# Performance work log

Measured on AMD Instinct MI355X. Metric: run time of the kernel, lower is better.

## Reference

```python
import jax, jax.numpy as jnp
import numpy as np

H = 4096
I = 11008
S = 4096
B = 1


def _swiglu_mlp(x, Wgu, Wd):
    # x: [B, T, H]; Wgu: [H, 2I]; Wd: [I, H]
    gu = jnp.einsum('bth,hi->bti', x, Wgu)
    gate, up = gu[..., :I], gu[..., I:]
    return jnp.einsum('bti,ih->bth', jax.nn.silu(gate) * up, Wd)


def setup_inputs() -> dict:
    key = jax.random.key(0)
    ks = jax.random.split(key, 5)
    scale_h = 1.0 / np.sqrt(H)
    scale_i = 1.0 / np.sqrt(I)
    hidden_states = jax.random.normal(ks[0], (B, S, H), dtype=jnp.float32)
    lang_ids = jnp.arange(S // 2, dtype=jnp.int64 if jax.config.jax_enable_x64 else jnp.int32)
    vision_ids = jnp.arange(S // 2, S, dtype=lang_ids.dtype)
    Wgu_lang = jax.random.normal(ks[1], (H, 2 * I), dtype=jnp.float32) * scale_h
    Wd_lang = jax.random.normal(ks[2], (I, H), dtype=jnp.float32) * scale_i
    Wgu_vis = jax.random.normal(ks[3], (H, 2 * I), dtype=jnp.float32) * scale_h
    Wd_vis = jax.random.normal(ks[4], (I, H), dtype=jnp.float32) * scale_i
    return {
        'hidden_states': hidden_states,
        'lang_ids': lang_ids,
        'vision_ids': vision_ids,
        'Wgu_lang': Wgu_lang,
        'Wd_lang': Wd_lang,
        'Wgu_vis': Wgu_vis,
        'Wd_vis': Wd_vis,
    }


def reference(hidden_states, lang_ids, vision_ids, Wgu_lang, Wd_lang, Wgu_vis, Wd_vis):
    # gather-by-token-type -> SwiGLU MLP per expert -> scatter-combine
    lang_out = _swiglu_mlp(hidden_states[:, lang_ids], Wgu_lang, Wd_lang)
    vis_out = _swiglu_mlp(hidden_states[:, vision_ids], Wgu_vis, Wd_vis)
    out = jnp.zeros_like(hidden_states)
    out = out.at[:, lang_ids].set(lang_out)
    out = out.at[:, vision_ids].set(vis_out)
    return out
```

## Files before the change

### kernel.cpp

```cpp
#include <hip/hip_runtime.h>
#include <hip/hip_bf16.h>


#define HDIM 4096
#define IDIM 11008
#define N2   22016
#define MTOK 2048
#define KT1  64
#define KT2  172
#define NB1  86
#define NB2  32
#define NKD  344
#define NPG  128

#define XPE_SH ((long)8 * KT1 * 16384)
#define WPE_SH ((long)NB1 * KT1 * 16384)
#define HPE_SH ((long)8 * KT2 * 16384)

typedef unsigned short ushort_t;
using f32x4  = __attribute__((ext_vector_type(4))) float;
using bf16x8 = __attribute__((ext_vector_type(8))) short;
using u32x2  = __attribute__((ext_vector_type(2))) unsigned int;
using u32x4  = __attribute__((ext_vector_type(4))) unsigned int;

__device__ __forceinline__ unsigned int bf16rne(float f) {
    unsigned int u = __builtin_bit_cast(unsigned int, f);
    return (u + 0x7FFFu + ((u >> 16) & 1u)) >> 16;
}
__device__ __forceinline__ unsigned int pack2(float lo, float hi) {
    return bf16rne(lo) | (bf16rne(hi) << 16);
}
__device__ __forceinline__ void gl_lds16(const void* g, void* l) {
    __builtin_amdgcn_global_load_lds(
        (const __attribute__((address_space(1))) void*)g,
        (__attribute__((address_space(3))) void*)l, 16, 0, 0);
}


__global__ __launch_bounds__(256)
void conv_x(const float* __restrict__ X, ushort_t* __restrict__ XP) {
    int bid = blockIdx.x;
    int mb = bid >> 6, kt = bid & 63;
    int t = threadIdx.x;
    int r0 = t >> 4, c4 = t & 15;
    int kh = c4 >> 3, c = (c4 >> 1) & 3, lo4 = (c4 & 1) << 2;
    ushort_t* tp = XP + ((long)(mb >> 1) * KT1 + kt) * 16384 + (long)kh * 8192 + (mb & 1) * 4096;
#pragma unroll
    for (int p = 0; p < 8; ++p) {
        int rl = r0 + p * 16;
        f32x4 v = *(const f32x4*)(X + (long)(mb * 128 + rl) * HDIM + kt * 64 + c4 * 4);
        u32x2 pk = { pack2(v[0], v[1]), pack2(v[2], v[3]) };
        int q = rl >> 1;
        int pos = ((((rl & 1) << 2) | c) ^ (q & 7));
        *(u32x2*)&tp[q * 64 + pos * 8 + lo4] = pk;
    }
}

__global__ __launch_bounds__(256)
void conv_wgu(const float* __restrict__ W, ushort_t* __restrict__ WP) {
    int bid = blockIdx.x;
    int e = bid & 1, kt = (bid >> 1) & 63, nb = bid >> 7;
    int t = threadIdx.x;
    int kp = t >> 5, c4 = t & 31;
    const float* p = W + ((long)kt * 64 + kp * 8) * N2 + (long)e * IDIM + nb * 128 + c4 * 4;
    f32x4 v[8];
#pragma unroll
    for (int j = 0; j < 8; ++j) v[j] = *(const f32x4*)(p + (long)j * N2);
    ushort_t* tp = WP + ((long)nb * KT1 + kt) * 16384 + (long)(kp >> 2) * 8192 + e * 4096;
    int c = kp & 3;
#pragma unroll
    for (int cc = 0; cc < 4; ++cc) {
        int n = c4 * 4 + cc;
        int q = n >> 1;
        int pos = ((((n & 1) << 2) | c) ^ (q & 7));
        u32x4 pk = { pack2(v[0][cc], v[1][cc]), pack2(v[2][cc], v[3][cc]),
                     pack2(v[4][cc], v[5][cc]), pack2(v[6][cc], v[7][cc]) };
        *(u32x4*)&tp[q * 64 + pos * 8] = pk;
    }
}

__global__ __launch_bounds__(256)
void conv_wd2b(const float* __restrict__ Wl, const float* __restrict__ Wv,
               ushort_t* __restrict__ WPd) {
    int bid = blockIdx.x;
    int kt = bid % KT2, nbp = bid / KT2;
    int e = nbp >> 4, nb = nbp & 15;
    const float* W = e ? Wv : Wl;
    int t = threadIdx.x;
    int kp = t >> 5, c4 = t & 31;
    ushort_t* tp = WPd + ((long)nbp * KT2 + kt) * 16384 + (long)(kp >> 2) * 8192;
    int c = kp & 3;
#pragma unroll
    for (int h = 0; h < 2; ++h) {
        const float* p = W + ((long)kt * 64 + kp * 8) * HDIM + nb * 256 + h * 128 + c4 * 4;
        f32x4 v[8];
#pragma unroll
        for (int j = 0; j < 8; ++j) v[j] = *(const f32x4*)(p + (long)j * HDIM);
#pragma unroll
        for (int cc = 0; cc < 4; ++cc) {
            int n = h * 128 + c4 * 4 + cc;
            int q = n >> 1;
            int pos = ((((n & 1) << 2) | c) ^ (q & 7));
            u32x4 pk = { pack2(v[0][cc], v[1][cc]), pack2(v[2][cc], v[3][cc]),
                         pack2(v[4][cc], v[5][cc]), pack2(v[6][cc], v[7][cc]) };
            *(u32x4*)&tp[q * 64 + pos * 8] = pk;
        }
    }
}

__global__ __launch_bounds__(256)
void conv_wd(const float* __restrict__ W, ushort_t* __restrict__ WP) {
    int bid = blockIdx.x;
    int kt = bid % KT2, nb = bid / KT2;
    int t = threadIdx.x;
    int kp = t >> 5, c4 = t & 31;
    const float* p = W + ((long)kt * 64 + kp * 8) * HDIM + nb * 128 + c4 * 4;
    f32x4 v[8];
#pragma unroll
    for (int j = 0; j < 8; ++j) v[j] = *(const f32x4*)(p + (long)j * HDIM);
    ushort_t* tp = WP + ((long)nb * KT2 + kt) * 8192 + (long)(kp >> 2) * 4096;
    int c = kp & 3;
#pragma unroll
    for (int cc = 0; cc < 4; ++cc) {
        int n = c4 * 4 + cc;
        int q = n >> 1;
        int pos = ((((n & 1) << 2) | c) ^ (q & 7));
        u32x4 pk = { pack2(v[0][cc], v[1][cc]), pack2(v[2][cc], v[3][cc]),
                     pack2(v[4][cc], v[5][cc]), pack2(v[6][cc], v[7][cc]) };
        *(u32x4*)&tp[q * 64 + pos * 8] = pk;
    }
}

#define STAGE_U(SRC, DSTOFF) do { \
    gl_lds16((SRC) + so + lane * 8, &lds[(DSTOFF) + so]); \
    gl_lds16((SRC) + 4096 + so + lane * 8, &lds[(DSTOFF) + 4096 + so]); } while (0)

#define MFMA16(ACC, AF, BF) \
    _Pragma("unroll") \
    for (int mf = 0; mf < 4; ++mf) \
        _Pragma("unroll") \
        for (int nf = 0; nf < 4; ++nf) \
            ACC[mf][nf] = __builtin_amdgcn_mfma_f32_16x16x32_bf16(AF[mf], BF[nf], ACC[mf][nf], 0, 0, 0);

#define VMCNT_MID(N) do { \
    if (pf) asm volatile("s_waitcnt vmcnt(" #N ")" ::: "memory"); \
    else    asm volatile("s_waitcnt vmcnt(0)" ::: "memory"); } while (0)
#define VMCNT_END(N) do { \
    if (pf) asm volatile("s_waitcnt vmcnt(" #N ")" ::: "memory"); } while (0)

__global__ __launch_bounds__(512, 2)
void gu15_kernel(const ushort_t* __restrict__ XP, const ushort_t* __restrict__ WP,
                 ushort_t* __restrict__ HP, int perE) {
    __shared__ ushort_t lds[49152];
    int nwg = gridDim.x;
    int cpx = nwg >> 3;
    int sw  = (blockIdx.x & 7) * cpx + (blockIdx.x >> 3);
    int e   = (sw >= perE) ? 1 : 0;
    int lsw = sw - e * perE;
    int mblk = lsw & 7;
    int nblk = lsw >> 3;
    const int t = threadIdx.x, lane = t & 63, w = t >> 6;
    const int wr = w >> 1, wc = w & 1;
    const int rr = lane & 15, g4 = lane >> 4;
    const int so = w * 512;

    int aoff[4], boff[4];
#pragma unroll
    for (int mf = 0; mf < 4; ++mf) {
        int m = wr * 64 + mf * 16 + rr, q = m >> 1;
        aoff[mf] = q * 64 + ((((((m & 1) << 2) | g4) ^ (q & 7))) << 3);
    }
#pragma unroll
    for (int nf = 0; nf < 4; ++nf) {
        int n = wc * 64 + nf * 16 + rr, q = n >> 1;
        boff[nf] = q * 64 + ((((((n & 1) << 2) | g4) ^ (q & 7))) << 3);
    }

    f32x4 accg[4][4] = {}, accu[4][4] = {};
    const ushort_t* srcA = XP + (long)e * XPE_SH + (long)mblk * KT1 * 16384;
    const ushort_t* srcB = WP + (long)e * WPE_SH + (long)nblk * KT1 * 16384;
    ushort_t* HPe = HP + (long)e * HPE_SH;

    STAGE_U(srcA, 0);
    STAGE_U(srcB, 8192);
    STAGE_U(srcA + 8192, 16384);
    STAGE_U(srcB + 8192, 16384 + 8192);
    asm volatile("s_waitcnt vmcnt(4)" ::: "memory");
    __builtin_amdgcn_s_barrier();

    int cb = 0, sb = 32768;
    for (int kt = 0; kt < NPG; ++kt) {
        bf16x8 af[4], bg[4], bu[4];
#pragma unroll
        for (int mf = 0; mf < 4; ++mf) af[mf] = *(const bf16x8*)&lds[cb + aoff[mf]];
#pragma unroll
        for (int nf = 0; nf < 4; ++nf) {
            bg[nf] = *(const bf16x8*)&lds[cb + 8192 + boff[nf]];
            bu[nf] = *(const bf16x8*)&lds[cb + 8192 + 4096 + boff[nf]];
        }
        const bool pf = (kt + 2 < NPG);
        if (pf) {
            const ushort_t* nA = srcA + (long)(kt + 2) * 8192;
            const ushort_t* nB = srcB + (long)(kt + 2) * 8192;
            STAGE_U(nA, sb);
            STAGE_U(nB, sb + 8192);
        }
        __builtin_amdgcn_s_setprio(1);
        MFMA16(accg, af, bg);
        MFMA16(accu, af, bu);
        __builtin_amdgcn_s_setprio(0);
        if (pf)                   asm volatile("s_waitcnt vmcnt(4)" ::: "memory");
        else if (kt + 1 < NPG)    asm volatile("s_waitcnt vmcnt(0)" ::: "memory");
        __builtin_amdgcn_s_barrier();
        sb = cb;
        cb += 16384; if (cb == 49152) cb = 0;
    }

#pragma unroll
    for (int nf = 0; nf < 4; ++nf) {
        int nloc = wc * 64 + nf * 16 + rr;
        int kt2 = nblk * 2 + (nloc >> 6);
        int k = nloc & 63;
        int kh = k >> 5, c = (k >> 3) & 3, klow = k & 7;
        ushort_t* tp = HPe + ((long)mblk * KT2 + kt2) * 16384 + kh * 8192 + klow;
#pragma unroll
        for (int mf = 0; mf < 4; ++mf)
#pragma unroll
            for (int i = 0; i < 4; ++i) {
                int m = wr * 64 + mf * 16 + g4 * 4 + i;
                int q = m >> 1;
                int pos = ((((m & 1) << 2) | c) ^ (q & 7));
                float gv = accg[mf][nf][i], uv = accu[mf][nf][i];
                float s = gv / (1.0f + __expf(-gv));
                tp[q * 64 + pos * 8] = (ushort_t)bf16rne(s * uv);
            }
    }
}

__global__ __launch_bounds__(512, 2)
void down6_kernel(const ushort_t* __restrict__ HP, const ushort_t* __restrict__ WPd,
                  float* __restrict__ Out) {
    __shared__ ushort_t lds[49152];
    int nwg = gridDim.x;
    int cpx = nwg >> 3;
    int sw  = (blockIdx.x & 7) * cpx + (blockIdx.x >> 3);
    int mblk = sw & 15;
    int nblk = sw >> 4;
    const int t = threadIdx.x, lane = t & 63, w = t >> 6;
    const int wr = w >> 2, wc = w & 3;
    const int rr = lane & 15, g4 = lane >> 4;
    const int so = w * 512;

    int aoff[8], boff[4];
#pragma unroll
    for (int mf = 0; mf < 8; ++mf) {
        int m = wr * 128 + mf * 16 + rr, q = m >> 1;
        aoff[mf] = q * 64 + ((((((m & 1) << 2) | g4) ^ (q & 7))) << 3);
    }
#pragma unroll
    for (int nf = 0; nf < 4; ++nf) {
        int n = wc * 64 + nf * 16 + rr, q = n >> 1;
        boff[nf] = q * 64 + ((((((n & 1) << 2) | g4) ^ (q & 7))) << 3);
    }

    f32x4 acc[8][4] = {};
    const ushort_t* srcA = HP  + (long)mblk * KT2 * 16384;
    const ushort_t* srcB = WPd + (long)(((mblk >> 3) << 4) + nblk) * KT2 * 16384;

    STAGE_U(srcA, 0);
    STAGE_U(srcB, 8192);
    STAGE_U(srcA + 8192, 16384);
    STAGE_U(srcB + 8192, 16384 + 8192);
    asm volatile("s_waitcnt vmcnt(4)" ::: "memory");
    __builtin_amdgcn_s_barrier();

    int cb = 0, sb = 32768;
    for (int kt = 0; kt < NKD; ++kt) {
        bf16x8 af[8], bf[4];
#pragma unroll
        for (int mf = 0; mf < 8; ++mf) af[mf] = *(const bf16x8*)&lds[cb + aoff[mf]];
#pragma unroll
        for (int nf = 0; nf < 4; ++nf) bf[nf] = *(const bf16x8*)&lds[cb + 8192 + boff[nf]];
        const bool pf = (kt + 2 < NKD);
        if (pf) {
            const ushort_t* nA = srcA + (long)(kt + 2) * 8192;
            const ushort_t* nB = srcB + (long)(kt + 2) * 8192;
            STAGE_U(nA, sb);
            STAGE_U(nB, sb + 8192);
        }
        __builtin_amdgcn_s_setprio(1);
#pragma unroll
        for (int mf = 0; mf < 8; ++mf)
#pragma unroll
            for (int nf = 0; nf < 4; ++nf)
                acc[mf][nf] = __builtin_amdgcn_mfma_f32_16x16x32_bf16(af[mf], bf[nf], acc[mf][nf], 0, 0, 0);
        __builtin_amdgcn_s_setprio(0);
        if (pf)                   asm volatile("s_waitcnt vmcnt(4)" ::: "memory");
        else if (kt + 1 < NKD)    asm volatile("s_waitcnt vmcnt(0)" ::: "memory");
        __builtin_amdgcn_s_barrier();
        sb = cb;
        cb += 16384; if (cb == 49152) cb = 0;
    }

#pragma unroll
    for (int mf = 0; mf < 8; ++mf)
#pragma unroll
        for (int nf = 0; nf < 4; ++nf)
#pragma unroll
            for (int i = 0; i < 4; ++i) {
                int m = mblk * 256 + wr * 128 + mf * 16 + g4 * 4 + i;
                int n = nblk * 256 + wc * 64 + nf * 16 + rr;
                Out[(long)m * HDIM + n] = acc[mf][nf][i];
            }
}

__global__ __launch_bounds__(512, 2)
void down3_kernel(const ushort_t* __restrict__ HP, const ushort_t* __restrict__ WP,
                  float* __restrict__ Out) {
    __shared__ ushort_t lds[49152];
    int nwg = gridDim.x;
    int cpx = nwg >> 3;
    int sw  = (blockIdx.x & 7) * cpx + (blockIdx.x >> 3);
    int mblk = sw & 7;
    int nblk = sw >> 3;
    const int t = threadIdx.x, lane = t & 63, w = t >> 6;
    const int wr = w >> 1, wc = w & 1;
    const int rr = lane & 15, g4 = lane >> 4;
    const int so = w * 512;

    int aoff[4], boff[4];
#pragma unroll
    for (int mf = 0; mf < 4; ++mf) {
        int m = wr * 64 + mf * 16 + rr, q = m >> 1;
        aoff[mf] = q * 64 + ((((((m & 1) << 2) | g4) ^ (q & 7))) << 3);
    }
#pragma unroll
    for (int nf = 0; nf < 4; ++nf) {
        int n = wc * 64 + nf * 16 + rr, q = n >> 1;
        boff[nf] = q * 64 + ((((((n & 1) << 2) | g4) ^ (q & 7))) << 3);
    }

    f32x4 acc[4][4] = {};
    const ushort_t* srcA = HP + (long)mblk * KT2 * 16384;
    const ushort_t* srcB = WP + (long)nblk * KT2 * 8192;

    STAGE_U(srcA, 0);
    STAGE_U(srcA + 8192, 8192);
    STAGE_U(srcB, 16384);
    asm volatile("s_waitcnt vmcnt(0)" ::: "memory");
    __builtin_amdgcn_s_barrier();

    int cur = 0;
    for (int kt = 0; kt < KT2; ++kt) {
        const int cb = cur * 24576, pb = (cur ^ 1) * 24576;
        const ushort_t* nA = srcA + (long)(kt + 1) * 16384;
        const ushort_t* nB = srcB + (long)(kt + 1) * 8192;
        const bool pf = (kt + 1 < KT2);
        bf16x8 af[4], bfr[4];

#pragma unroll
        for (int mf = 0; mf < 4; ++mf) af[mf] = *(const bf16x8*)&lds[cb + aoff[mf]];
#pragma unroll
        for (int nf = 0; nf < 4; ++nf) bfr[nf] = *(const bf16x8*)&lds[cb + 16384 + boff[nf]];
        if (pf) { STAGE_U(nA, pb); STAGE_U(nB, pb + 16384); }
        __builtin_amdgcn_s_barrier();
        __builtin_amdgcn_s_setprio(1);
        MFMA16(acc, af, bfr);
        __builtin_amdgcn_s_setprio(0);
        VMCNT_MID(4);
        __builtin_amdgcn_s_barrier();

#pragma unroll
        for (int mf = 0; mf < 4; ++mf) af[mf] = *(const bf16x8*)&lds[cb + 8192 + aoff[mf]];
#pragma unroll
        for (int nf = 0; nf < 4; ++nf) bfr[nf] = *(const bf16x8*)&lds[cb + 20480 + boff[nf]];
        if (pf) STAGE_U(nA + 8192, pb + 8192);
        __builtin_amdgcn_s_barrier();
        __builtin_amdgcn_s_setprio(1);
        MFMA16(acc, af, bfr);
        __builtin_amdgcn_s_setprio(0);
        VMCNT_END(2);
        __builtin_amdgcn_s_barrier();

        cur ^= 1;
    }

#pragma unroll
    for (int mf = 0; mf < 4; ++mf)
#pragma unroll
        for (int nf = 0; nf < 4; ++nf)
#pragma unroll
            for (int i = 0; i < 4; ++i) {
                int m = mblk * 256 + wr * 64 + mf * 16 + g4 * 4 + i;
                int n = nblk * 128 + wc * 64 + nf * 16 + rr;
                Out[(long)m * HDIM + n] = acc[mf][nf][i];
            }
}

extern "C" void kernel_launch(void* const* d_in, const int* in_sizes, int n_in,
                              void* d_out, int out_size, void* d_ws, size_t ws_size,
                              hipStream_t stream) {
    const float* x     = (const float*)d_in[0];
    const float* Wgu_l = (const float*)d_in[3];
    const float* Wd_l  = (const float*)d_in[4];
    const float* Wgu_v = (const float*)d_in[5];
    const float* Wd_v  = (const float*)d_in[6];
    float* out         = (float*)d_out;

    const size_t XP_B  = (size_t)8 * KT1 * 32768;
    const size_t HP_B  = (size_t)8 * KT2 * 32768;
    const size_t WP_B  = (size_t)NB1 * KT1 * 32768;
    const size_t NEED0 = 2 * XP_B + 2 * HP_B + 2 * WP_B;
    const size_t NEED1 = XP_B + 2 * HP_B + WP_B;

    if (ws_size >= NEED0) {
        ushort_t* XP = (ushort_t*)d_ws;
        ushort_t* HP = XP + 2 * XPE_SH;
        ushort_t* WP = HP + 2 * HPE_SH;
        for (int e = 0; e < 2; ++e) {
            conv_x  <<<dim3(16 * KT1),      dim3(256), 0, stream>>>(
                x + (long)e * MTOK * HDIM, XP + (long)e * XPE_SH);
            conv_wgu<<<dim3(NB1 * KT1 * 2), dim3(256), 0, stream>>>(
                e ? Wgu_v : Wgu_l, WP + (long)e * WPE_SH);
        }
        gu15_kernel<<<dim3(16 * NB1), dim3(512), 0, stream>>>(XP, WP, HP, 8 * NB1);
        conv_wd2b<<<dim3(32 * KT2), dim3(256), 0, stream>>>(Wd_l, Wd_v, WP);
        down6_kernel<<<dim3(256), dim3(512), 0, stream>>>(HP, WP, out);
    } else if (ws_size >= NEED1) {
        ushort_t* XP = (ushort_t*)d_ws;
        ushort_t* HP = XP + XPE_SH;
        ushort_t* WP = HP + 2 * HPE_SH;
        for (int e = 0; e < 2; ++e) {
            conv_x  <<<dim3(16 * KT1),      dim3(256), 0, stream>>>(
                x + (long)e * MTOK * HDIM, XP);
            conv_wgu<<<dim3(NB1 * KT1 * 2), dim3(256), 0, stream>>>(
                e ? Wgu_v : Wgu_l, WP);
            gu15_kernel<<<dim3(8 * NB1), dim3(512), 0, stream>>>(
                XP, WP, HP + (long)e * HPE_SH, 8 * NB1);
        }
        conv_wd2b<<<dim3(32 * KT2), dim3(256), 0, stream>>>(Wd_l, Wd_v, WP);
        down6_kernel<<<dim3(256), dim3(512), 0, stream>>>(HP, WP, out);
    } else {
        ushort_t* XP = (ushort_t*)d_ws;
        ushort_t* HP = XP + XPE_SH;
        ushort_t* WP = HP + HPE_SH;
        for (int e = 0; e < 2; ++e) {
            const float* xe = x + (long)e * MTOK * HDIM;
            float*       oe = out + (long)e * MTOK * HDIM;
            conv_x  <<<dim3(16 * KT1),      dim3(256), 0, stream>>>(xe, XP);
            conv_wgu<<<dim3(NB1 * KT1 * 2), dim3(256), 0, stream>>>(e ? Wgu_v : Wgu_l, WP);
            gu15_kernel<<<dim3(8 * NB1),    dim3(512), 0, stream>>>(XP, WP, HP, 8 * NB1);
            conv_wd <<<dim3(NB2 * KT2),     dim3(256), 0, stream>>>(e ? Wd_v : Wd_l, WP);
            down3_kernel<<<dim3(8 * NB2),   dim3(512), 0, stream>>>(HP, WP, oe);
        }
    }
}
```

Measured before the change: 1.228 ms.

## Switch GEMM pipelines to double-buffered two-subtile stages with half the barriers

The gate-up and down GEMM kernels move from a 3-slot ring of 32-wide K subtiles (one barrier per subtile, prefetch depth 2) to two 64-wide K buffers. Each loop iteration computes two subtiles, prefetches the next full tile into the other buffer, then waits with vmcnt(0) and a barrier. This halves the number of barriers and waitcnt points. The cost is more LDS per block (128KB), which could lower occupancy, and a shallower prefetch distance, which gives less latency hiding.

Result: slower. 1.254 ms (+2.1%).

```diff
diff --git a/kernel.cpp b/kernel.cpp
--- a/kernel.cpp
+++ b/kernel.cpp
@@ -10,8 +10,6 @@
 #define KT2  172
 #define NB1  86
 #define NB2  32
-#define NKD  344
-#define NPG  128
 
 #define XPE_SH ((long)8 * KT1 * 16384)
 #define WPE_SH ((long)NB1 * KT1 * 16384)
@@ -135,6 +133,12 @@
     gl_lds16((SRC) + so + lane * 8, &lds[(DSTOFF) + so]); \
     gl_lds16((SRC) + 4096 + so + lane * 8, &lds[(DSTOFF) + 4096 + so]); } while (0)
 
+#define STAGE_TILE(NA, NB, PB) do { \
+    STAGE_U((NA), (PB)); \
+    STAGE_U((NB), (PB) + 8192); \
+    STAGE_U((NA) + 8192, (PB) + 16384); \
+    STAGE_U((NB) + 8192, (PB) + 24576); } while (0)
+
 #define MFMA16(ACC, AF, BF) \
     _Pragma("unroll") \
     for (int mf = 0; mf < 4; ++mf) \
@@ -149,9 +153,9 @@
     if (pf) asm volatile("s_waitcnt vmcnt(" #N ")" ::: "memory"); } while (0)
 
 __global__ __launch_bounds__(512, 2)
-void gu15_kernel(const ushort_t* __restrict__ XP, const ushort_t* __restrict__ WP,
+void gu16_kernel(const ushort_t* __restrict__ XP, const ushort_t* __restrict__ WP,
                  ushort_t* __restrict__ HP, int perE) {
-    __shared__ ushort_t lds[49152];
+    __shared__ ushort_t lds[65536];
     int nwg = gridDim.x;
     int cpx = nwg >> 3;
     int sw  = (blockIdx.x & 7) * cpx + (blockIdx.x >> 3);
@@ -181,16 +185,15 @@
     const ushort_t* srcB = WP + (long)e * WPE_SH + (long)nblk * KT1 * 16384;
     ushort_t* HPe = HP + (long)e * HPE_SH;
 
-    STAGE_U(srcA, 0);
-    STAGE_U(srcB, 8192);
-    STAGE_U(srcA + 8192, 16384);
-    STAGE_U(srcB + 8192, 16384 + 8192);
-    asm volatile("s_waitcnt vmcnt(4)" ::: "memory");
+    STAGE_TILE(srcA, srcB, 0);
+    asm volatile("s_waitcnt vmcnt(0)" ::: "memory");
     __builtin_amdgcn_s_barrier();
 
-    int cb = 0, sb = 32768;
-    for (int kt = 0; kt < NPG; ++kt) {
+    for (int tt = 0; tt < KT1; ++tt) {
+        const int cb = (tt & 1) << 15;
+        const int pb = cb ^ 32768;
         bf16x8 af[4], bg[4], bu[4];
+
 #pragma unroll
         for (int mf = 0; mf < 4; ++mf) af[mf] = *(const bf16x8*)&lds[cb + aoff[mf]];
 #pragma unroll
@@ -198,22 +201,30 @@
             bg[nf] = *(const bf16x8*)&lds[cb + 8192 + boff[nf]];
             bu[nf] = *(const bf16x8*)&lds[cb + 8192 + 4096 + boff[nf]];
         }
-        const bool pf = (kt + 2 < NPG);
-        if (pf) {
-            const ushort_t* nA = srcA + (long)(kt + 2) * 8192;
-            const ushort_t* nB = srcB + (long)(kt + 2) * 8192;
-            STAGE_U(nA, sb);
-            STAGE_U(nB, sb + 8192);
+        if (tt + 1 < KT1) {
+            const ushort_t* nA = srcA + (long)(tt + 1) * 16384;
+            const ushort_t* nB = srcB + (long)(tt + 1) * 16384;
+            STAGE_TILE(nA, nB, pb);
         }
         __builtin_amdgcn_s_setprio(1);
         MFMA16(accg, af, bg);
         MFMA16(accu, af, bu);
         __builtin_amdgcn_s_setprio(0);
-        if (pf)                   asm volatile("s_waitcnt vmcnt(4)" ::: "memory");
-        else if (kt + 1 < NPG)    asm volatile("s_waitcnt vmcnt(0)" ::: "memory");
-        __builtin_amdgcn_s_barrier();
-        sb = cb;
-        cb += 16384; if (cb == 49152) cb = 0;
+
+#pragma unroll
+        for (int mf = 0; mf < 4; ++mf) af[mf] = *(const bf16x8*)&lds[cb + 16384 + aoff[mf]];
+#pragma unroll
+        for (int nf = 0; nf < 4; ++nf) {
+            bg[nf] = *(const bf16x8*)&lds[cb + 24576 + boff[nf]];
+            bu[nf] = *(const bf16x8*)&lds[cb + 24576 + 4096 + boff[nf]];
+        }
+        __builtin_amdgcn_s_setprio(1);
+        MFMA16(accg, af, bg);
+        MFMA16(accu, af, bu);
+        __builtin_amdgcn_s_setprio(0);
+
+        asm volatile("s_waitcnt vmcnt(0)" ::: "memory");
+        __builtin_amdgcn_s_barrier();
     }
 
 #pragma unroll
@@ -238,9 +249,9 @@
 }
 
 __global__ __launch_bounds__(512, 2)
-void down6_kernel(const ushort_t* __restrict__ HP, const ushort_t* __restrict__ WPd,
+void down8_kernel(const ushort_t* __restrict__ HP, const ushort_t* __restrict__ WPd,
                   float* __restrict__ Out) {
-    __shared__ ushort_t lds[49152];
+    __shared__ ushort_t lds[65536];
     int nwg = gridDim.x;
     int cpx = nwg >> 3;
     int sw  = (blockIdx.x & 7) * cpx + (blockIdx.x >> 3);
@@ -267,26 +278,23 @@
     const ushort_t* srcA = HP  + (long)mblk * KT2 * 16384;
     const ushort_t* srcB = WPd + (long)(((mblk >> 3) << 4) + nblk) * KT2 * 16384;
 
-    STAGE_U(srcA, 0);
-    STAGE_U(srcB, 8192);
-    STAGE_U(srcA + 8192, 16384);
-    STAGE_U(srcB + 8192, 16384 + 8192);
-    asm volatile("s_waitcnt vmcnt(4)" ::: "memory");
+    STAGE_TILE(srcA, srcB, 0);
+    asm volatile("s_waitcnt vmcnt(0)" ::: "memory");
     __builtin_amdgcn_s_barrier();
 
-    int cb = 0, sb = 32768;
-    for (int kt = 0; kt < NKD; ++kt) {
+    for (int tt = 0; tt < KT2; ++tt) {
+        const int cb = (tt & 1) << 15;
+        const int pb = cb ^ 32768;
         bf16x8 af[8], bf[4];
+
 #pragma unroll
         for (int mf = 0; mf < 8; ++mf) af[mf] = *(const bf16x8*)&lds[cb + aoff[mf]];
 #pragma unroll
         for (int nf = 0; nf < 4; ++nf) bf[nf] = *(const bf16x8*)&lds[cb + 8192 + boff[nf]];
-        const bool pf = (kt + 2 < NKD);
-        if (pf) {
-            const ushort_t* nA = srcA + (long)(kt + 2) * 8192;
-            const ushort_t* nB = srcB + (long)(kt + 2) * 8192;
-            STAGE_U(nA, sb);
-            STAGE_U(nB, sb + 8192);
+        if (tt + 1 < KT2) {
+            const ushort_t* nA = srcA + (long)(tt + 1) * 16384;
+            const ushort_t* nB = srcB + (long)(tt + 1) * 16384;
+            STAGE_TILE(nA, nB, pb);
         }
         __builtin_amdgcn_s_setprio(1);
 #pragma unroll
@@ -295,11 +303,21 @@
             for (int nf = 0; nf < 4; ++nf)
                 acc[mf][nf] = __builtin_amdgcn_mfma_f32_16x16x32_bf16(af[mf], bf[nf], acc[mf][nf], 0, 0, 0);
         __builtin_amdgcn_s_setprio(0);
-        if (pf)                   asm volatile("s_waitcnt vmcnt(4)" ::: "memory");
-        else if (kt + 1 < NKD)    asm volatile("s_waitcnt vmcnt(0)" ::: "memory");
-        __builtin_amdgcn_s_barrier();
-        sb = cb;
-        cb += 16384; if (cb == 49152) cb = 0;
+
+#pragma unroll
+        for (int mf = 0; mf < 8; ++mf) af[mf] = *(const bf16x8*)&lds[cb + 16384 + aoff[mf]];
+#pragma unroll
+        for (int nf = 0; nf < 4; ++nf) bf[nf] = *(const bf16x8*)&lds[cb + 24576 + boff[nf]];
+        __builtin_amdgcn_s_setprio(1);
+#pragma unroll
+        for (int mf = 0; mf < 8; ++mf)
+#pragma unroll
+            for (int nf = 0; nf < 4; ++nf)
+                acc[mf][nf] = __builtin_amdgcn_mfma_f32_16x16x32_bf16(af[mf], bf[nf], acc[mf][nf], 0, 0, 0);
+        __builtin_amdgcn_s_setprio(0);
+
+        asm volatile("s_waitcnt vmcnt(0)" ::: "memory");
+        __builtin_amdgcn_s_barrier();
     }
 
 #pragma unroll
@@ -423,9 +441,9 @@
             conv_wgu<<<dim3(NB1 * KT1 * 2), dim3(256), 0, stream>>>(
                 e ? Wgu_v : Wgu_l, WP + (long)e * WPE_SH);
         }
-        gu15_kernel<<<dim3(16 * NB1), dim3(512), 0, stream>>>(XP, WP, HP, 8 * NB1);
+        gu16_kernel<<<dim3(16 * NB1), dim3(512), 0, stream>>>(XP, WP, HP, 8 * NB1);
         conv_wd2b<<<dim3(32 * KT2), dim3(256), 0, stream>>>(Wd_l, Wd_v, WP);
-        down6_kernel<<<dim3(256), dim3(512), 0, stream>>>(HP, WP, out);
+        down8_kernel<<<dim3(256), dim3(512), 0, stream>>>(HP, WP, out);
     } else if (ws_size >= NEED1) {
         ushort_t* XP = (ushort_t*)d_ws;
         ushort_t* HP = XP + XPE_SH;
@@ -435,11 +453,11 @@
                 x + (long)e * MTOK * HDIM, XP);
             conv_wgu<<<dim3(NB1 * KT1 * 2), dim3(256), 0, stream>>>(
                 e ? Wgu_v : Wgu_l, WP);
-            gu15_kernel<<<dim3(8 * NB1), dim3(512), 0, stream>>>(
+            gu16_kernel<<<dim3(8 * NB1), dim3(512), 0, stream>>>(
                 XP, WP, HP + (long)e * HPE_SH, 8 * NB1);
         }
         conv_wd2b<<<dim3(32 * KT2), dim3(256), 0, stream>>>(Wd_l, Wd_v, WP);
-        down6_kernel<<<dim3(256), dim3(512), 0, stream>>>(HP, WP, out);
+        down8_kernel<<<dim3(256), dim3(512), 0, stream>>>(HP, WP, out);
     } else {
         ushort_t* XP = (ushort_t*)d_ws;
         ushort_t* HP = XP + XPE_SH;
@@ -449,7 +467,7 @@
             float*       oe = out + (long)e * MTOK * HDIM;
             conv_x  <<<dim3(16 * KT1),      dim3(256), 0, stream>>>(xe, XP);
             conv_wgu<<<dim3(NB1 * KT1 * 2), dim3(256), 0, stream>>>(e ? Wgu_v : Wgu_l, WP);
-            gu15_kernel<<<dim3(8 * NB1),    dim3(512), 0, stream>>>(XP, WP, HP, 8 * NB1);
+            gu16_kernel<<<dim3(8 * NB1),    dim3(512), 0, stream>>>(XP, WP, HP, 8 * NB1);
             conv_wd <<<dim3(NB2 * KT2),     dim3(256), 0, stream>>>(e ? Wd_v : Wd_l, WP);
             down3_kernel<<<dim3(8 * NB2),   dim3(512), 0, stream>>>(HP, WP, oe);
         }
```

## Deepen LDS pipeline to four stages with register double-buffered fragments

Applied to the files above, without the earlier changes.

Both the gate/up GEMM and the down-projection GEMM move from a three-buffer LDS ring to a four-buffer ring, prefetching three k-tiles ahead instead of two. The loop is unrolled by two, and the operand fragments for the next k-step are read from LDS into a second register set while the current step's MFMAs run, which overlaps LDS reads with matrix math. In exchange, LDS per block grows from 96 KB to 128 KB and register pressure rises, so fewer blocks may fit per CU than the launch bounds request.

Measured after the change: 1.250 ms. No clear change (+1.8%).

```diff
diff --git a/kernel.cpp b/kernel.cpp
--- a/kernel.cpp
+++ b/kernel.cpp
@@ -148,10 +148,32 @@
 #define VMCNT_END(N) do { \
     if (pf) asm volatile("s_waitcnt vmcnt(" #N ")" ::: "memory"); } while (0)
 
+#define GU_STEP(KT, CA, CG, CU, NA_, NG_, NU_) do { \
+    if ((KT) + 1 < NPG) { \
+        const int rbs = (((KT) + 1) & 3) << 14; \
+        _Pragma("unroll") for (int mf = 0; mf < 4; ++mf) NA_[mf] = *(const bf16x8*)&lds[rbs + aoff[mf]]; \
+        _Pragma("unroll") for (int nf = 0; nf < 4; ++nf) { \
+            NG_[nf] = *(const bf16x8*)&lds[rbs + 8192 + boff[nf]]; \
+            NU_[nf] = *(const bf16x8*)&lds[rbs + 12288 + boff[nf]]; } \
+    } \
+    if ((KT) + 3 < NPG) { \
+        const int ssb = (((KT) + 3) & 3) << 14; \
+        STAGE_U(srcA + (long)((KT) + 3) * 8192, ssb); \
+        STAGE_U(srcB + (long)((KT) + 3) * 8192, ssb + 8192); \
+    } \
+    __builtin_amdgcn_s_setprio(1); \
+    MFMA16(accg, CA, CG); \
+    MFMA16(accu, CA, CU); \
+    __builtin_amdgcn_s_setprio(0); \
+    if ((KT) + 3 < NPG)      asm volatile("s_waitcnt vmcnt(4)" ::: "memory"); \
+    else if ((KT) + 2 < NPG) asm volatile("s_waitcnt vmcnt(0)" ::: "memory"); \
+    __builtin_amdgcn_s_barrier(); \
+} while (0)
+
 __global__ __launch_bounds__(512, 2)
-void gu15_kernel(const ushort_t* __restrict__ XP, const ushort_t* __restrict__ WP,
+void gu17_kernel(const ushort_t* __restrict__ XP, const ushort_t* __restrict__ WP,
                  ushort_t* __restrict__ HP, int perE) {
-    __shared__ ushort_t lds[49152];
+    __shared__ ushort_t lds[65536];
     int nwg = gridDim.x;
     int cpx = nwg >> 3;
     int sw  = (blockIdx.x & 7) * cpx + (blockIdx.x >> 3);
@@ -181,39 +203,24 @@
     const ushort_t* srcB = WP + (long)e * WPE_SH + (long)nblk * KT1 * 16384;
     ushort_t* HPe = HP + (long)e * HPE_SH;
 
-    STAGE_U(srcA, 0);
-    STAGE_U(srcB, 8192);
-    STAGE_U(srcA + 8192, 16384);
-    STAGE_U(srcB + 8192, 16384 + 8192);
+    STAGE_U(srcA, 0);                 STAGE_U(srcB, 8192);
+    STAGE_U(srcA + 8192, 16384);      STAGE_U(srcB + 8192, 16384 + 8192);
+    STAGE_U(srcA + 16384, 32768);     STAGE_U(srcB + 16384, 32768 + 8192);
     asm volatile("s_waitcnt vmcnt(4)" ::: "memory");
     __builtin_amdgcn_s_barrier();
 
-    int cb = 0, sb = 32768;
-    for (int kt = 0; kt < NPG; ++kt) {
-        bf16x8 af[4], bg[4], bu[4];
-#pragma unroll
-        for (int mf = 0; mf < 4; ++mf) af[mf] = *(const bf16x8*)&lds[cb + aoff[mf]];
-#pragma unroll
-        for (int nf = 0; nf < 4; ++nf) {
-            bg[nf] = *(const bf16x8*)&lds[cb + 8192 + boff[nf]];
-            bu[nf] = *(const bf16x8*)&lds[cb + 8192 + 4096 + boff[nf]];
-        }
-        const bool pf = (kt + 2 < NPG);
-        if (pf) {
-            const ushort_t* nA = srcA + (long)(kt + 2) * 8192;
-            const ushort_t* nB = srcB + (long)(kt + 2) * 8192;
-            STAGE_U(nA, sb);
-            STAGE_U(nB, sb + 8192);
-        }
-        __builtin_amdgcn_s_setprio(1);
-        MFMA16(accg, af, bg);
-        MFMA16(accu, af, bu);
-        __builtin_amdgcn_s_setprio(0);
-        if (pf)                   asm volatile("s_waitcnt vmcnt(4)" ::: "memory");
-        else if (kt + 1 < NPG)    asm volatile("s_waitcnt vmcnt(0)" ::: "memory");
-        __builtin_amdgcn_s_barrier();
-        sb = cb;
-        cb += 16384; if (cb == 49152) cb = 0;
+    bf16x8 afA[4], bgA[4], buA[4], afB[4], bgB[4], buB[4];
+#pragma unroll
+    for (int mf = 0; mf < 4; ++mf) afA[mf] = *(const bf16x8*)&lds[aoff[mf]];
+#pragma unroll
+    for (int nf = 0; nf < 4; ++nf) {
+        bgA[nf] = *(const bf16x8*)&lds[8192 + boff[nf]];
+        buA[nf] = *(const bf16x8*)&lds[12288 + boff[nf]];
+    }
+
+    for (int kt = 0; kt < NPG; kt += 2) {
+        GU_STEP(kt,     afA, bgA, buA, afB, bgB, buB);
+        GU_STEP(kt + 1, afB, bgB, buB, afA, bgA, buA);
     }
 
 #pragma unroll
@@ -237,10 +244,31 @@
     }
 }
 
+#define DN_STEP(KT, CA, CB, NA_, NB_) do { \
+    if ((KT) + 1 < NKD) { \
+        const int rbs = (((KT) + 1) & 3) << 14; \
+        _Pragma("unroll") for (int mf = 0; mf < 8; ++mf) NA_[mf] = *(const bf16x8*)&lds[rbs + aoff[mf]]; \
+        _Pragma("unroll") for (int nf = 0; nf < 4; ++nf) NB_[nf] = *(const bf16x8*)&lds[rbs + 8192 + boff[nf]]; \
+    } \
+    if ((KT) + 3 < NKD) { \
+        const int ssb = (((KT) + 3) & 3) << 14; \
+        STAGE_U(srcA + (long)((KT) + 3) * 8192, ssb); \
+        STAGE_U(srcB + (long)((KT) + 3) * 8192, ssb + 8192); \
+    } \
+    __builtin_amdgcn_s_setprio(1); \
+    _Pragma("unroll") for (int mf = 0; mf < 8; ++mf) \
+        _Pragma("unroll") for (int nf = 0; nf < 4; ++nf) \
+            acc[mf][nf] = __builtin_amdgcn_mfma_f32_16x16x32_bf16(CA[mf], CB[nf], acc[mf][nf], 0, 0, 0); \
+    __builtin_amdgcn_s_setprio(0); \
+    if ((KT) + 3 < NKD)      asm volatile("s_waitcnt vmcnt(4)" ::: "memory"); \
+    else if ((KT) + 2 < NKD) asm volatile("s_waitcnt vmcnt(0)" ::: "memory"); \
+    __builtin_amdgcn_s_barrier(); \
+} while (0)
+
 __global__ __launch_bounds__(512, 2)
-void down6_kernel(const ushort_t* __restrict__ HP, const ushort_t* __restrict__ WPd,
+void down9_kernel(const ushort_t* __restrict__ HP, const ushort_t* __restrict__ WPd,
                   float* __restrict__ Out) {
-    __shared__ ushort_t lds[49152];
+    __shared__ ushort_t lds[65536];
     int nwg = gridDim.x;
     int cpx = nwg >> 3;
     int sw  = (blockIdx.x & 7) * cpx + (blockIdx.x >> 3);
@@ -267,39 +295,21 @@
     const ushort_t* srcA = HP  + (long)mblk * KT2 * 16384;
     const ushort_t* srcB = WPd + (long)(((mblk >> 3) << 4) + nblk) * KT2 * 16384;
 
-    STAGE_U(srcA, 0);
-    STAGE_U(srcB, 8192);
-    STAGE_U(srcA + 8192, 16384);
-    STAGE_U(srcB + 8192, 16384 + 8192);
+    STAGE_U(srcA, 0);                 STAGE_U(srcB, 8192);
+    STAGE_U(srcA + 8192, 16384);      STAGE_U(srcB + 8192, 16384 + 8192);
+    STAGE_U(srcA + 16384, 32768);     STAGE_U(srcB + 16384, 32768 + 8192);
     asm volatile("s_waitcnt vmcnt(4)" ::: "memory");
     __builtin_amdgcn_s_barrier();
 
-    int cb = 0, sb = 32768;
-    for (int kt = 0; kt < NKD; ++kt) {
-        bf16x8 af[8], bf[4];
-#pragma unroll
-        for (int mf = 0; mf < 8; ++mf) af[mf] = *(const bf16x8*)&lds[cb + aoff[mf]];
-#pragma unroll
-        for (int nf = 0; nf < 4; ++nf) bf[nf] = *(const bf16x8*)&lds[cb + 8192 + boff[nf]];
-        const bool pf = (kt + 2 < NKD);
-        if (pf) {
-            const ushort_t* nA = srcA + (long)(kt + 2) * 8192;
-            const ushort_t* nB = srcB + (long)(kt + 2) * 8192;
-            STAGE_U(nA, sb);
-            STAGE_U(nB, sb + 8192);
-        }
-        __builtin_amdgcn_s_setprio(1);
-#pragma unroll
-        for (int mf = 0; mf < 8; ++mf)
-#pragma unroll
-            for (int nf = 0; nf < 4; ++nf)
-                acc[mf][nf] = __builtin_amdgcn_mfma_f32_16x16x32_bf16(af[mf], bf[nf], acc[mf][nf], 0, 0, 0);
-        __builtin_amdgcn_s_setprio(0);
-        if (pf)                   asm volatile("s_waitcnt vmcnt(4)" ::: "memory");
-        else if (kt + 1 < NKD)    asm volatile("s_waitcnt vmcnt(0)" ::: "memory");
-        __builtin_amdgcn_s_barrier();
-        sb = cb;
-        cb += 16384; if (cb == 49152) cb = 0;
+    bf16x8 afA[8], bfA[4], afB[8], bfB[4];
+#pragma unroll
+    for (int mf = 0; mf < 8; ++mf) afA[mf] = *(const bf16x8*)&lds[aoff[mf]];
+#pragma unroll
+    for (int nf = 0; nf < 4; ++nf) bfA[nf] = *(const bf16x8*)&lds[8192 + boff[nf]];
+
+    for (int kt = 0; kt < NKD; kt += 2) {
+        DN_STEP(kt,     afA, bfA, afB, bfB);
+        DN_STEP(kt + 1, afB, bfB, afA, bfA);
     }
 
 #pragma unroll
@@ -423,9 +433,9 @@
             conv_wgu<<<dim3(NB1 * KT1 * 2), dim3(256), 0, stream>>>(
                 e ? Wgu_v : Wgu_l, WP + (long)e * WPE_SH);
         }
-        gu15_kernel<<<dim3(16 * NB1), dim3(512), 0, stream>>>(XP, WP, HP, 8 * NB1);
+        gu17_kernel<<<dim3(16 * NB1), dim3(512), 0, stream>>>(XP, WP, HP, 8 * NB1);
         conv_wd2b<<<dim3(32 * KT2), dim3(256), 0, stream>>>(Wd_l, Wd_v, WP);
-        down6_kernel<<<dim3(256), dim3(512), 0, stream>>>(HP, WP, out);
+        down9_kernel<<<dim3(256), dim3(512), 0, stream>>>(HP, WP, out);
     } else if (ws_size >= NEED1) {
         ushort_t* XP = (ushort_t*)d_ws;
         ushort_t* HP = XP + XPE_SH;
@@ -435,11 +445,11 @@
                 x + (long)e * MTOK * HDIM, XP);
             conv_wgu<<<dim3(NB1 * KT1 * 2), dim3(256), 0, stream>>>(
                 e ? Wgu_v : Wgu_l, WP);
-            gu15_kernel<<<dim3(8 * NB1), dim3(512), 0, stream>>>(
+            gu17_kernel<<<dim3(8 * NB1), dim3(512), 0, stream>>>(
                 XP, WP, HP + (long)e * HPE_SH, 8 * NB1);
         }
         conv_wd2b<<<dim3(32 * KT2), dim3(256), 0, stream>>>(Wd_l, Wd_v, WP);
-        down6_kernel<<<dim3(256), dim3(512), 0, stream>>>(HP, WP, out);
+        down9_kernel<<<dim3(256), dim3(512), 0, stream>>>(HP, WP, out);
     } else {
         ushort_t* XP = (ushort_t*)d_ws;
         ushort_t* HP = XP + XPE_SH;
@@ -449,7 +459,7 @@
             float*       oe = out + (long)e * MTOK * HDIM;
             conv_x  <<<dim3(16 * KT1),      dim3(256), 0, stream>>>(xe, XP);
             conv_wgu<<<dim3(NB1 * KT1 * 2), dim3(256), 0, stream>>>(e ? Wgu_v : Wgu_l, WP);
-            gu15_kernel<<<dim3(8 * NB1),    dim3(512), 0, stream>>>(XP, WP, HP, 8 * NB1);
+            gu17_kernel<<<dim3(8 * NB1),    dim3(512), 0, stream>>>(XP, WP, HP, 8 * NB1);
             conv_wd <<<dim3(NB2 * KT2),     dim3(256), 0, stream>>>(e ? Wd_v : Wd_l, WP);
             down3_kernel<<<dim3(8 * NB2),   dim3(512), 0, stream>>>(HP, WP, oe);
         }
```

## Fold next-stage weight conversion into tail of gate-up GEMM kernels

Applied to the files above, without the earlier changes.

Splits the combined two-expert gate/up GEMM launch into two per-expert launches. After its GEMM epilogue, each workgroup converts a slice of the next stage's weights to packed bf16: the vision Wgu during the language GEMM, and both down-projection weights during the vision GEMM. This removes the standalone conversion launches and hides memory-bound conversion work behind compute-bound GEMM tails. It adds register pressure and extra epilogue time to the GEMM kernel, and gives up the single larger launch that covered both experts.

Result: no change. 1.215 ms (-1.0%).

```diff
diff --git a/kernel.cpp b/kernel.cpp
--- a/kernel.cpp
+++ b/kernel.cpp
@@ -37,6 +37,55 @@
 }
 
 
+__device__ __forceinline__ void conv_wgu_unit(const float* __restrict__ W,
+                                              ushort_t* __restrict__ WP, int bid, int t) {
+    int e = bid & 1, kt = (bid >> 1) & 63, nb = bid >> 7;
+    int kp = t >> 5, c4 = t & 31;
+    const float* p = W + ((long)kt * 64 + kp * 8) * N2 + (long)e * IDIM + nb * 128 + c4 * 4;
+    f32x4 v[8];
+#pragma unroll
+    for (int j = 0; j < 8; ++j) v[j] = *(const f32x4*)(p + (long)j * N2);
+    ushort_t* tp = WP + ((long)nb * KT1 + kt) * 16384 + (long)(kp >> 2) * 8192 + e * 4096;
+    int c = kp & 3;
+#pragma unroll
+    for (int cc = 0; cc < 4; ++cc) {
+        int n = c4 * 4 + cc;
+        int q = n >> 1;
+        int pos = ((((n & 1) << 2) | c) ^ (q & 7));
+        u32x4 pk = { pack2(v[0][cc], v[1][cc]), pack2(v[2][cc], v[3][cc]),
+                     pack2(v[4][cc], v[5][cc]), pack2(v[6][cc], v[7][cc]) };
+        *(u32x4*)&tp[q * 64 + pos * 8] = pk;
+    }
+}
+
+__device__ __forceinline__ void conv_wd2b_unit(const float* __restrict__ Wl,
+                                               const float* __restrict__ Wv,
+                                               ushort_t* __restrict__ WPd, int bid, int t) {
+    int kt = bid % KT2, nbp = bid / KT2;
+    int e = nbp >> 4, nb = nbp & 15;
+    const float* W = e ? Wv : Wl;
+    int kp = t >> 5, c4 = t & 31;
+    ushort_t* tp = WPd + ((long)nbp * KT2 + kt) * 16384 + (long)(kp >> 2) * 8192;
+    int c = kp & 3;
+#pragma unroll
+    for (int h = 0; h < 2; ++h) {
+        const float* p = W + ((long)kt * 64 + kp * 8) * HDIM + nb * 256 + h * 128 + c4 * 4;
+        f32x4 v[8];
+#pragma unroll
+        for (int j = 0; j < 8; ++j) v[j] = *(const f32x4*)(p + (long)j * HDIM);
+#pragma unroll
+        for (int cc = 0; cc < 4; ++cc) {
+            int n = h * 128 + c4 * 4 + cc;
+            int q = n >> 1;
+            int pos = ((((n & 1) << 2) | c) ^ (q & 7));
+            u32x4 pk = { pack2(v[0][cc], v[1][cc]), pack2(v[2][cc], v[3][cc]),
+                         pack2(v[4][cc], v[5][cc]), pack2(v[6][cc], v[7][cc]) };
+            *(u32x4*)&tp[q * 64 + pos * 8] = pk;
+        }
+    }
+}
+
+
 __global__ __launch_bounds__(256)
 void conv_x(const float* __restrict__ X, ushort_t* __restrict__ XP) {
     int bid = blockIdx.x;
@@ -58,54 +107,13 @@
 
 __global__ __launch_bounds__(256)
 void conv_wgu(const float* __restrict__ W, ushort_t* __restrict__ WP) {
-    int bid = blockIdx.x;
-    int e = bid & 1, kt = (bid >> 1) & 63, nb = bid >> 7;
-    int t = threadIdx.x;
-    int kp = t >> 5, c4 = t & 31;
-    const float* p = W + ((long)kt * 64 + kp * 8) * N2 + (long)e * IDIM + nb * 128 + c4 * 4;
-    f32x4 v[8];
-#pragma unroll
-    for (int j = 0; j < 8; ++j) v[j] = *(const f32x4*)(p + (long)j * N2);
-    ushort_t* tp = WP + ((long)nb * KT1 + kt) * 16384 + (long)(kp >> 2) * 8192 + e * 4096;
-    int c = kp & 3;
-#pragma unroll
-    for (int cc = 0; cc < 4; ++cc) {
-        int n = c4 * 4 + cc;
-        int q = n >> 1;
-        int pos = ((((n & 1) << 2) | c) ^ (q & 7));
-        u32x4 pk = { pack2(v[0][cc], v[1][cc]), pack2(v[2][cc], v[3][cc]),
-                     pack2(v[4][cc], v[5][cc]), pack2(v[6][cc], v[7][cc]) };
-        *(u32x4*)&tp[q * 64 + pos * 8] = pk;
-    }
+    conv_wgu_unit(W, WP, blockIdx.x, threadIdx.x);
 }
 
 __global__ __launch_bounds__(256)
 void conv_wd2b(const float* __restrict__ Wl, const float* __restrict__ Wv,
                ushort_t* __restrict__ WPd) {
-    int bid = blockIdx.x;
-    int kt = bid % KT2, nbp = bid / KT2;
-    int e = nbp >> 4, nb = nbp & 15;
-    const float* W = e ? Wv : Wl;
-    int t = threadIdx.x;
-    int kp = t >> 5, c4 = t & 31;
-    ushort_t* tp = WPd + ((long)nbp * KT2 + kt) * 16384 + (long)(kp >> 2) * 8192;
-    int c = kp & 3;
-#pragma unroll
-    for (int h = 0; h < 2; ++h) {
-        const float* p = W + ((long)kt * 64 + kp * 8) * HDIM + nb * 256 + h * 128 + c4 * 4;
-        f32x4 v[8];
-#pragma unroll
-        for (int j = 0; j < 8; ++j) v[j] = *(const f32x4*)(p + (long)j * HDIM);
-#pragma unroll
-        for (int cc = 0; cc < 4; ++cc) {
-            int n = h * 128 + c4 * 4 + cc;
-            int q = n >> 1;
-            int pos = ((((n & 1) << 2) | c) ^ (q & 7));
-            u32x4 pk = { pack2(v[0][cc], v[1][cc]), pack2(v[2][cc], v[3][cc]),
-                         pack2(v[4][cc], v[5][cc]), pack2(v[6][cc], v[7][cc]) };
-            *(u32x4*)&tp[q * 64 + pos * 8] = pk;
-        }
-    }
+    conv_wd2b_unit(Wl, Wv, WPd, blockIdx.x, threadIdx.x);
 }
 
 __global__ __launch_bounds__(256)
@@ -149,16 +157,16 @@
     if (pf) asm volatile("s_waitcnt vmcnt(" #N ")" ::: "memory"); } while (0)
 
 __global__ __launch_bounds__(512, 2)
-void gu15_kernel(const ushort_t* __restrict__ XP, const ushort_t* __restrict__ WP,
-                 ushort_t* __restrict__ HP, int perE) {
+void gu18_kernel(const ushort_t* __restrict__ XPe, const ushort_t* __restrict__ WPe,
+                 ushort_t* __restrict__ HPe, int convMode,
+                 const float* __restrict__ cwA, const float* __restrict__ cwB,
+                 ushort_t* __restrict__ cdst) {
     __shared__ ushort_t lds[49152];
     int nwg = gridDim.x;
     int cpx = nwg >> 3;
     int sw  = (blockIdx.x & 7) * cpx + (blockIdx.x >> 3);
-    int e   = (sw >= perE) ? 1 : 0;
-    int lsw = sw - e * perE;
-    int mblk = lsw & 7;
-    int nblk = lsw >> 3;
+    int mblk = sw & 7;
+    int nblk = sw >> 3;
     const int t = threadIdx.x, lane = t & 63, w = t >> 6;
     const int wr = w >> 1, wc = w & 1;
     const int rr = lane & 15, g4 = lane >> 4;
@@ -177,9 +185,8 @@
     }
 
     f32x4 accg[4][4] = {}, accu[4][4] = {};
-    const ushort_t* srcA = XP + (long)e * XPE_SH + (long)mblk * KT1 * 16384;
-    const ushort_t* srcB = WP + (long)e * WPE_SH + (long)nblk * KT1 * 16384;
-    ushort_t* HPe = HP + (long)e * HPE_SH;
+    const ushort_t* srcA = XPe + (long)mblk * KT1 * 16384;
+    const ushort_t* srcB = WPe + (long)nblk * KT1 * 16384;
 
     STAGE_U(srcA, 0);
     STAGE_U(srcB, 8192);
@@ -234,6 +241,20 @@
                 float s = gv / (1.0f + __expf(-gv));
                 tp[q * 64 + pos * 8] = (ushort_t)bf16rne(s * uv);
             }
+    }
+
+    if (convMode == 1) {
+        int tl = t & 255, half = t >> 8;
+        int base = sw * 16;
+#pragma unroll 2
+        for (int i = 0; i < 8; ++i)
+            conv_wgu_unit(cwA, cdst, base + i * 2 + half, tl);
+    } else if (convMode == 2) {
+        int tl = t & 255, half = t >> 8;
+        int base = sw * 8;
+#pragma unroll 2
+        for (int i = 0; i < 4; ++i)
+            conv_wd2b_unit(cwA, cwB, cdst, base + i * 2 + half, tl);
     }
 }
 
@@ -417,14 +438,13 @@
         ushort_t* XP = (ushort_t*)d_ws;
         ushort_t* HP = XP + 2 * XPE_SH;
         ushort_t* WP = HP + 2 * HPE_SH;
-        for (int e = 0; e < 2; ++e) {
-            conv_x  <<<dim3(16 * KT1),      dim3(256), 0, stream>>>(
-                x + (long)e * MTOK * HDIM, XP + (long)e * XPE_SH);
-            conv_wgu<<<dim3(NB1 * KT1 * 2), dim3(256), 0, stream>>>(
-                e ? Wgu_v : Wgu_l, WP + (long)e * WPE_SH);
-        }
-        gu15_kernel<<<dim3(16 * NB1), dim3(512), 0, stream>>>(XP, WP, HP, 8 * NB1);
-        conv_wd2b<<<dim3(32 * KT2), dim3(256), 0, stream>>>(Wd_l, Wd_v, WP);
+        conv_x  <<<dim3(16 * KT1),      dim3(256), 0, stream>>>(x, XP);
+        conv_x  <<<dim3(16 * KT1),      dim3(256), 0, stream>>>(x + (long)MTOK * HDIM, XP + XPE_SH);
+        conv_wgu<<<dim3(NB1 * KT1 * 2), dim3(256), 0, stream>>>(Wgu_l, WP);
+        gu18_kernel<<<dim3(8 * NB1), dim3(512), 0, stream>>>(
+            XP, WP, HP, 1, Wgu_v, nullptr, WP + WPE_SH);
+        gu18_kernel<<<dim3(8 * NB1), dim3(512), 0, stream>>>(
+            XP + XPE_SH, WP + WPE_SH, HP + HPE_SH, 2, Wd_l, Wd_v, WP);
         down6_kernel<<<dim3(256), dim3(512), 0, stream>>>(HP, WP, out);
     } else if (ws_size >= NEED1) {
         ushort_t* XP = (ushort_t*)d_ws;
@@ -435,8 +455,8 @@
                 x + (long)e * MTOK * HDIM, XP);
             conv_wgu<<<dim3(NB1 * KT1 * 2), dim3(256), 0, stream>>>(
                 e ? Wgu_v : Wgu_l, WP);
-            gu15_kernel<<<dim3(8 * NB1), dim3(512), 0, stream>>>(
-                XP, WP, HP + (long)e * HPE_SH, 8 * NB1);
+            gu18_kernel<<<dim3(8 * NB1), dim3(512), 0, stream>>>(
+                XP, WP, HP + (long)e * HPE_SH, 0, nullptr, nullptr, nullptr);
         }
         conv_wd2b<<<dim3(32 * KT2), dim3(256), 0, stream>>>(Wd_l, Wd_v, WP);
         down6_kernel<<<dim3(256), dim3(512), 0, stream>>>(HP, WP, out);
@@ -449,7 +469,8 @@
             float*       oe = out + (long)e * MTOK * HDIM;
             conv_x  <<<dim3(16 * KT1),      dim3(256), 0, stream>>>(xe, XP);
             conv_wgu<<<dim3(NB1 * KT1 * 2), dim3(256), 0, stream>>>(e ? Wgu_v : Wgu_l, WP);
-            gu15_kernel<<<dim3(8 * NB1),    dim3(512), 0, stream>>>(XP, WP, HP, 8 * NB1);
+            gu18_kernel<<<dim3(8 * NB1),    dim3(512), 0, stream>>>(
+                XP, WP, HP, 0, nullptr, nullptr, nullptr);
             conv_wd <<<dim3(NB2 * KT2),     dim3(256), 0, stream>>>(e ? Wd_v : Wd_l, WP);
             down3_kernel<<<dim3(8 * NB2),   dim3(512), 0, stream>>>(HP, WP, oe);
         }
```
